# Optimization experiments

Hardware: AMD Instinct MI355X
Metric: run time of the kernel (lower is better)

## Reference

```python
import jax, jax.numpy as jnp
import numpy as np

NUM_BATCH = 8  # GroupNormalization(num_batch=num_groups) with num_groups=8
EPS = 1e-6


def setup_inputs() -> dict:
    key = jax.random.key(0)
    k1, k2, k3 = jax.random.split(key, 3)
    b, h, w, c = 32, 32, 32, 256
    x = jax.random.normal(k1, (b, h, w, c), dtype=jnp.float32)
    gamma = jnp.ones((c,), dtype=jnp.float32)
    beta = jnp.zeros((c,), dtype=jnp.float32)
    w_qkv = jax.random.normal(k2, (c, 3 * c), dtype=jnp.float32) * 0.02
    w_out = jax.random.normal(k3, (c, c), dtype=jnp.float32) * 0.02
    return {"x": x, "gamma": gamma, "beta": beta, "w_qkv": w_qkv, "w_out": w_out}


def reference(x, gamma, beta, w_qkv, w_out):
    b, h, w, c = x.shape
    # --- GroupNormalization (exact quirky semantics of the source) ---
    # num_groups = c // num_batch; reshape to [-1, num_groups, group_size]
    # -> per-(b,h,w)-pixel normalization over contiguous channel groups.
    ng = c // NUM_BATCH          # 32 groups
    gs = c // ng                 # 8 channels per group
    g = x.reshape(-1, ng, gs)
    mu = jnp.mean(g, axis=-1, keepdims=True)
    var = jnp.mean(jnp.square(g - mu), axis=-1, keepdims=True)
    xn = ((g - mu) / jnp.sqrt(var + EPS)).reshape(x.shape)
    xn = gamma * xn + beta
    # --- 1x1 conv to qkv (bias-free) ---
    qkv = jnp.einsum('bhwc,cd->bhwd', xn, w_qkv)  # [b,h,w,3c]
    q, k, v = jnp.split(qkv, 3, axis=-1)
    # self_attention=True branch: tie q=k=v to their mean
    t = (v + q + k) / 3.0
    q = k = v = t
    # --- exact reshapes from the source (raw reshapes, not transposes) ---
    q = jnp.transpose(q, (0, 3, 1, 2)).reshape(b, h * w, c)  # [b,hw,c]
    k = k.reshape(b, c, h * w)                               # [b,c,hw]
    v = jnp.transpose(v, (0, 3, 1, 2)).reshape(b, h * w, c)  # [b,hw,c]
    scores = jnp.matmul(q, k) * (c ** -0.5)                  # [b,hw,hw]
    attn = jax.nn.softmax(scores, axis=-1)
    # NOTE: source passes transpose_a=float (truthy) -> attention is transposed
    out = jnp.matmul(jnp.swapaxes(attn, 1, 2), v)            # [b,hw,c]
    out = out.reshape(b, h, w, c)
    return jnp.einsum('bhwc,cd->bhwd', out, w_out) + x
```

## Files before the change

### kernel.cpp

```cpp
#include <hip/hip_runtime.h>

typedef unsigned short u16;
typedef unsigned char u8;
typedef long long i64;
typedef __bf16 bf16x8 __attribute__((ext_vector_type(8)));
typedef float f32x4 __attribute__((ext_vector_type(4)));
typedef u16 u16x8 __attribute__((ext_vector_type(8)));

#define GLD16(g, l) __builtin_amdgcn_global_load_lds( \
    (const __attribute__((address_space(1))) void*)(g), \
    (__attribute__((address_space(3))) void*)(l), 16, 0, 0)

__device__ __forceinline__ float bf2f(u16 u) {
  return __uint_as_float(((unsigned)u) << 16);
}
__device__ __forceinline__ u16 f2bf(float f) {
  unsigned u = __float_as_uint(f);
  return (u16)((u + 0x7fffu + ((u >> 16) & 1u)) >> 16);
}
__device__ __forceinline__ u8 f8e_sw(float v) {
  unsigned u = __float_as_uint(v);
  unsigned s = (u >> 24) & 0x80u;
  u &= 0x7fffffffu;
  if (u < 0x3c000000u) return (u8)s;
  int b = (int)((u + 0x7FFFFu + ((u >> 20) & 1u)) >> 20) - 960;
  b = b < 8 ? 8 : (b > 126 ? 126 : b);
  return (u8)(b | s);
}
__device__ __forceinline__ float f8d_sw(u8 b) {
  if (!(b & 0x7f)) return 0.0f;
  float v = __uint_as_float((((unsigned)(b & 0x7fu)) << 20) + 0x3C000000u);
  return (b & 0x80u) ? -v : v;
}
__device__ __forceinline__ unsigned pk4(float a, float b, float c, float d) {
#if __has_builtin(__builtin_amdgcn_cvt_pk_fp8_f32)
  int r = __builtin_amdgcn_cvt_pk_fp8_f32(a, b, 0, false);
  r = __builtin_amdgcn_cvt_pk_fp8_f32(c, d, r, true);
  return (unsigned)r;
#else
  return (unsigned)f8e_sw(a) | ((unsigned)f8e_sw(b) << 8) |
         ((unsigned)f8e_sw(c) << 16) | ((unsigned)f8e_sw(d) << 24);
#endif
}
__device__ __forceinline__ float f8df(u8 b) {
#if __has_builtin(__builtin_amdgcn_cvt_f32_fp8)
  return __builtin_amdgcn_cvt_f32_fp8((int)b, 0);
#else
  return f8d_sw(b);
#endif
}
__device__ __forceinline__ int sig(int r) { return (r ^ (r >> 3)) & 7; }

__global__ void combine_w(const float* __restrict__ wqkv, const float* __restrict__ wout,
                          u16* __restrict__ wtT, u16* __restrict__ woutT) {
  int c = blockIdx.x, d = threadIdx.x;
  float t = (wqkv[c * 768 + d] + wqkv[c * 768 + 256 + d] + wqkv[c * 768 + 512 + d]) * (1.0f / 3.0f);
  wtT[d * 256 + c] = f2bf(t);
  woutT[d * 256 + c] = f2bf(wout[c * 256 + d]);
}

__global__ __launch_bounds__(512) void gnT(
    const float* __restrict__ x, const float* __restrict__ gamma,
    const float* __restrict__ beta, const u16* __restrict__ wtT,
    u8* __restrict__ Q8, u8* __restrict__ Kt8) {
  __shared__ u16 lA[2][64 * 64];
  __shared__ u16 lB[2][256 * 64];
  const int m0 = blockIdx.x * 64;
  const int z = m0 >> 10;
  const int t = threadIdx.x, lane = t & 63;
  const int w = t >> 6, wr = w >> 2, wc = w & 3;
  f32x4 acc[2][4] = {};

#define GNT_STAGE(B, K0)                                                        \
  {                                                                             \
    _Pragma("unroll") for (int ch = 0; ch < 4; ch++) {                          \
      int flat = ch * 512 + t, row = flat >> 3, slot = flat & 7;                \
      GLD16(wtT + (size_t)row * 256 + (K0) + (slot ^ sig(row)) * 8,             \
            lB[B] + flat * 8);                                                  \
    }                                                                           \
    int row = t >> 3, grp = t & 7;                                              \
    const float* xp = x + (size_t)(m0 + row) * 256 + (K0) + grp * 8;            \
    float4 a = *(const float4*)xp, b = *(const float4*)(xp + 4);                \
    float mu = (a.x + a.y + a.z + a.w + b.x + b.y + b.z + b.w) * 0.125f;        \
    float d0 = a.x - mu, d1 = a.y - mu, d2 = a.z - mu, d3 = a.w - mu;           \
    float d4 = b.x - mu, d5 = b.y - mu, d6 = b.z - mu, d7 = b.w - mu;           \
    float var = (d0 * d0 + d1 * d1 + d2 * d2 + d3 * d3 +                        \
                 d4 * d4 + d5 * d5 + d6 * d6 + d7 * d7) * 0.125f;               \
    float rs = rsqrtf(var + 1e-6f);                                             \
    const float4 g0 = *(const float4*)(gamma + (K0) + grp * 8);                 \
    const float4 g1 = *(const float4*)(gamma + (K0) + grp * 8 + 4);             \
    const float4 e0 = *(const float4*)(beta + (K0) + grp * 8);                  \
    const float4 e1 = *(const float4*)(beta + (K0) + grp * 8 + 4);              \
    u16x8 o;                                                                    \
    o[0] = f2bf(g0.x * (d0 * rs) + e0.x); o[1] = f2bf(g0.y * (d1 * rs) + e0.y); \
    o[2] = f2bf(g0.z * (d2 * rs) + e0.z); o[3] = f2bf(g0.w * (d3 * rs) + e0.w); \
    o[4] = f2bf(g1.x * (d4 * rs) + e1.x); o[5] = f2bf(g1.y * (d5 * rs) + e1.y); \
    o[6] = f2bf(g1.z * (d6 * rs) + e1.z); o[7] = f2bf(g1.w * (d7 * rs) + e1.w); \
    *(u16x8*)(lA[B] + row * 64 + (grp ^ sig(row)) * 8) = o;                     \
  }

  GNT_STAGE(0, 0);
  __syncthreads();
  for (int it = 0; it < 4; it++) {
    if (it < 3) { GNT_STAGE((it + 1) & 1, (it + 1) * 64); }
    const u16* la = lA[it & 1];
    const u16* lb = lB[it & 1];
#pragma unroll
    for (int kk = 0; kk < 2; kk++) {
      bf16x8 af[2], bfr[4];
#pragma unroll
      for (int mi = 0; mi < 2; mi++) {
        int m = wr * 32 + mi * 16 + (lane & 15);
        af[mi] = *(const bf16x8*)(la + m * 64 + ((kk * 32 + (lane >> 4) * 8) ^ (sig(m) << 3)));
      }
#pragma unroll
      for (int ni = 0; ni < 4; ni++) {
        int n = wc * 64 + ni * 16 + (lane & 15);
        bfr[ni] = *(const bf16x8*)(lb + n * 64 + ((kk * 32 + (lane >> 4) * 8) ^ (sig(n) << 3)));
      }
#pragma unroll
      for (int mi = 0; mi < 2; mi++)
#pragma unroll
        for (int ni = 0; ni < 4; ni++)
          acc[mi][ni] = __builtin_amdgcn_mfma_f32_16x16x32_bf16(af[mi], bfr[ni], acc[mi][ni], 0, 0, 0);
    }
    __syncthreads();
  }

  const int rb = m0 + wr * 32 + ((lane >> 4) << 2);
  const int cb = wc * 64 + (lane & 15);
  u8* kt = (u8*)lB[0];
  u8* qtile = (u8*)lB[1];
#pragma unroll
  for (int mi = 0; mi < 2; mi++)
#pragma unroll
    for (int ni = 0; ni < 4; ni++) {
      int P0 = rb + mi * 16, c = cb + ni * 16;
      int pl = P0 - m0;
      unsigned pk = pk4(acc[mi][ni][0], acc[mi][ni][1], acc[mi][ni][2], acc[mi][ni][3]);
#pragma unroll
      for (int j = 0; j < 4; j++)
        kt[(j * 256 + c) * 16 + (pl >> 2)] = (u8)(pk >> (8 * j));
      *(unsigned*)(qtile + c * 80 + pl) = pk;
    }
  __syncthreads();
  const int ckb = (m0 & 1023) >> 2;
  u8* Kz = Kt8 + (size_t)z * 262144;
  u8* Qz = Q8 + (size_t)z * 262144;
#pragma unroll
  for (int r2 = 0; r2 < 2; r2++) {
    int r = t * 2 + r2;
    uint4 v = *(const uint4*)(kt + r * 16);
    *(uint4*)(Kz + (size_t)r * 256 + ckb) = v;
  }
#pragma unroll
  for (int ph = 0; ph < 2; ph++) {
    int idx = ph * 512 + t, c = idx >> 2, q = idx & 3;
    uint4 v = *(const uint4*)(qtile + c * 80 + q * 16);
    *(uint4*)(Qz + (size_t)c * 1024 + (m0 & 1023) + q * 16) = v;
  }
#undef GNT_STAGE
}

__global__ __launch_bounds__(256) void gemm_s8(
    const u8* __restrict__ Q8, const u8* __restrict__ Kt8,
    u8* __restrict__ Et, float* __restrict__ partials) {
  __shared__ u8 lA[128 * 256];
  __shared__ u8 lB[128 * 256];
  const int z = blockIdx.z;
  const u8* Az = Q8 + (size_t)z * 262144;
  const u8* Bz = Kt8 + (size_t)z * 262144;
  u8* Ez = Et + (size_t)z * 1048576;
  const int m0 = blockIdx.x * 128, n0 = blockIdx.y * 128;
  const int t = threadIdx.x, lane = t & 63;
  const int wr = (t >> 6) >> 1, wc = (t >> 6) & 1;
  f32x4 acc[4][4] = {};

#pragma unroll
  for (int ch = 0; ch < 8; ch++) {
    int flat = ch * 256 + t, row = flat >> 4, slot = flat & 15;
    GLD16(Az + (size_t)(m0 + row) * 256 + (slot ^ sig(row)) * 16, lA + flat * 16);
  }
#pragma unroll
  for (int ch = 0; ch < 8; ch++) {
    int flat = ch * 256 + t, row = flat >> 4, slot = flat & 15;
    GLD16(Bz + (size_t)(n0 + row) * 256 + (slot ^ sig(row)) * 16, lB + flat * 16);
  }
  __syncthreads();
#pragma unroll
  for (int kk = 0; kk < 8; kk++) {
    i64 af[4], bfv[4];
    int koff = kk * 32 + (lane >> 4) * 8;
#pragma unroll
    for (int mi = 0; mi < 4; mi++) {
      int m = wr * 64 + mi * 16 + (lane & 15);
      af[mi] = *(const i64*)(lA + m * 256 + (koff ^ (sig(m) << 4)));
    }
#pragma unroll
    for (int ni = 0; ni < 4; ni++) {
      int n = wc * 64 + ni * 16 + (lane & 15);
      bfv[ni] = *(const i64*)(lB + n * 256 + (koff ^ (sig(n) << 4)));
    }
#pragma unroll
    for (int mi = 0; mi < 4; mi++)
#pragma unroll
      for (int ni = 0; ni < 4; ni++)
        acc[mi][ni] = __builtin_amdgcn_mfma_f32_16x16x32_fp8_fp8(af[mi], bfv[ni], acc[mi][ni], 0, 0, 0);
  }
  __syncthreads();
  u8* ldsC = lA;
  const int rbl = wr * 64 + ((lane >> 4) << 2);
  const int cbl = wc * 64 + (lane & 15);
  const float SCL = 0.0625f * 1.44269504089f;
  float ps[4][4] = {};
#pragma unroll
  for (int mi = 0; mi < 4; mi++)
#pragma unroll
    for (int ni = 0; ni < 4; ni++) {
      int pl = cbl + ni * 16, ib = rbl + mi * 16;
      float e0 = exp2f(acc[mi][ni][0] * SCL);
      float e1 = exp2f(acc[mi][ni][1] * SCL);
      float e2 = exp2f(acc[mi][ni][2] * SCL);
      float e3 = exp2f(acc[mi][ni][3] * SCL);
      ps[mi][0] += e0; ps[mi][1] += e1; ps[mi][2] += e2; ps[mi][3] += e3;
      *(unsigned*)(ldsC + pl * 128 + (ib ^ ((pl & 7) << 4))) = pk4(e0, e1, e2, e3);
    }
#pragma unroll
  for (int mi = 0; mi < 4; mi++)
#pragma unroll
    for (int j = 0; j < 4; j++) {
      float v = ps[mi][j];
      v += __shfl_xor(v, 1); v += __shfl_xor(v, 2);
      v += __shfl_xor(v, 4); v += __shfl_xor(v, 8);
      if ((lane & 15) == 0)
        partials[(size_t)(z * 1024 + m0 + rbl + mi * 16 + j) * 16 + blockIdx.y * 2 + wc] = v;
    }
  __syncthreads();
#pragma unroll
  for (int ph = 0; ph < 4; ph++) {
    int pl = ph * 32 + (t >> 3), ich = (t & 7) * 16;
    uint4 v = *(const uint4*)(ldsC + pl * 128 + (ich ^ ((pl & 7) << 4)));
    *(uint4*)(Ez + (size_t)(n0 + pl) * 1024 + m0 + ich) = v;
  }
}

__global__ __launch_bounds__(256) void qt8(
    const u8* __restrict__ Q8, const float* __restrict__ partials, u8* __restrict__ Qt) {
  __shared__ u8 tile[64][260];
  __shared__ float rv[64];
  const int z = blockIdx.y, i0 = blockIdx.x * 64;
  const u8* src = Q8 + (size_t)z * 262144;
  u8* dst = Qt + (size_t)z * 262144;
  const int t = threadIdx.x;
#pragma unroll
  for (int q = 0; q < 4; q++) {
    uint4 v = *(const uint4*)(src + (size_t)(i0 + (t >> 2)) * 256 + (t & 3) * 64 + q * 16);
    *(uint4*)(&tile[t >> 2][(t & 3) * 64 + q * 16]) = v;
  }
  if (t < 64) {
    const float4* p = (const float4*)(partials + (size_t)(z * 1024 + i0 + t) * 16);
    float4 a = p[0], b = p[1], c = p[2], d = p[3];
    float s = ((a.x + a.y) + (a.z + a.w)) + ((b.x + b.y) + (b.z + b.w)) +
              ((c.x + c.y) + (c.z + c.w)) + ((d.x + d.y) + (d.z + d.w));
    rv[t] = 1024.0f / s;
  }
  __syncthreads();
#pragma unroll
  for (int q = 0; q < 4; q++) {
    unsigned wd[4];
#pragma unroll
    for (int d = 0; d < 4; d++) {
      float f[4];
#pragma unroll
      for (int e = 0; e < 4; e++) {
        int i = q * 16 + d * 4 + e;
        f[e] = f8df(tile[i][t]) * rv[i];
      }
      wd[d] = pk4(f[0], f[1], f[2], f[3]);
    }
    uint4 v = {wd[0], wd[1], wd[2], wd[3]};
    *(uint4*)(dst + (size_t)t * 1024 + i0 + q * 16) = v;
  }
}

__global__ __launch_bounds__(512) void gemm_of(
    const u8* __restrict__ Et, const u8* __restrict__ Qt,
    const u16* __restrict__ woutT, const float* __restrict__ x,
    float* __restrict__ C) {
  __shared__ char smem[131072];
  const int z = blockIdx.y;
  const u8* Az = Et + (size_t)z * 1048576;
  const u8* Bz = Qt + (size_t)z * 262144;
  const int m0 = blockIdx.x * 128;
  const int t = threadIdx.x, lane = t & 63;
  const int w = t >> 6, wr = w >> 2, wc = w & 3;
  f32x4 acc[4][4] = {};

#define O8_STAGE(B, K0)                                                       \
  {                                                                           \
    u8* la_ = (u8*)smem + (B) * 16384;                                        \
    u8* lb_ = (u8*)smem + 32768 + (B) * 32768;                                \
    _Pragma("unroll") for (int ch = 0; ch < 2; ch++) {                        \
      int flat = ch * 512 + t, row = flat >> 3, slot = flat & 7;              \
      GLD16(Az + (size_t)(m0 + row) * 1024 + (K0) + (slot ^ sig(row)) * 16,   \
            la_ + flat * 16);                                                 \
    }                                                                         \
    _Pragma("unroll") for (int ch = 0; ch < 4; ch++) {                        \
      int flat = ch * 512 + t, row = flat >> 3, slot = flat & 7;              \
      GLD16(Bz + (size_t)row * 1024 + (K0) + (slot ^ sig(row)) * 16,          \
            lb_ + flat * 16);                                                 \
    }                                                                         \
  }

  O8_STAGE(0, 0);
  __syncthreads();
  for (int it = 0; it < 8; it++) {
    if (it < 7) { O8_STAGE((it + 1) & 1, (it + 1) * 128); }
    const u8* la = (const u8*)smem + (it & 1) * 16384;
    const u8* lb = (const u8*)smem + 32768 + (it & 1) * 32768;
#pragma unroll
    for (int kk = 0; kk < 4; kk++) {
      i64 af[4], bfv[4];
      int koff = kk * 32 + (lane >> 4) * 8;
#pragma unroll
      for (int mi = 0; mi < 4; mi++) {
        int m = wr * 64 + mi * 16 + (lane & 15);
        af[mi] = *(const i64*)(la + m * 128 + (koff ^ (sig(m) << 4)));
      }
#pragma unroll
      for (int ni = 0; ni < 4; ni++) {
        int n = wc * 64 + ni * 16 + (lane & 15);
        bfv[ni] = *(const i64*)(lb + n * 128 + (koff ^ (sig(n) << 4)));
      }
#pragma unroll
      for (int mi = 0; mi < 4; mi++)
#pragma unroll
        for (int ni = 0; ni < 4; ni++)
          acc[mi][ni] = __builtin_amdgcn_mfma_f32_16x16x32_fp8_fp8(af[mi], bfv[ni], acc[mi][ni], 0, 0, 0);
    }
    __syncthreads();
  }
#undef O8_STAGE

#define W_STAGE(B, K0)                                                        \
  {                                                                           \
    u16* wb_ = (u16*)(smem + 65536 + (B) * 32768);                            \
    _Pragma("unroll") for (int ch = 0; ch < 4; ch++) {                        \
      int flat = ch * 512 + t, row = flat >> 3, slot = flat & 7;              \
      GLD16(woutT + (size_t)row * 256 + (K0) + (slot ^ sig(row)) * 8,         \
            (u8*)wb_ + flat * 16);                                            \
    }                                                                         \
  }
  W_STAGE(0, 0);
  {
    const int rbl = wr * 64 + ((lane >> 4) << 2);
    const int cbl = wc * 64 + (lane & 15);
#pragma unroll
    for (int mi = 0; mi < 4; mi++)
#pragma unroll
      for (int ni = 0; ni < 4; ni++)
#pragma unroll
        for (int j = 0; j < 4; j++) {
          int pl = rbl + mi * 16 + j, c = cbl + ni * 16;
          int byteoff = (pl * 512 + c * 2) ^ ((pl & 7) << 4);
          *(u16*)(smem + byteoff) = f2bf(acc[mi][ni][j] * (1.0f / 1024.0f));
        }
  }
  __syncthreads();

  f32x4 acc2[4][4] = {};
  for (int it2 = 0; it2 < 4; it2++) {
    if (it2 < 3) { W_STAGE((it2 + 1) & 1, (it2 + 1) * 64); }
    const u16* lb = (const u16*)(smem + 65536 + (it2 & 1) * 32768);
#pragma unroll
    for (int kk = 0; kk < 2; kk++) {
      bf16x8 af[4], bfr[4];
#pragma unroll
      for (int mi = 0; mi < 4; mi++) {
        int m = wr * 64 + mi * 16 + (lane & 15);
        int kg = it2 * 64 + kk * 32 + (lane >> 4) * 8;
        af[mi] = *(const bf16x8*)(smem + ((m * 512 + kg * 2) ^ ((m & 7) << 4)));
      }
#pragma unroll
      for (int ni = 0; ni < 4; ni++) {
        int n = wc * 64 + ni * 16 + (lane & 15);
        bfr[ni] = *(const bf16x8*)(lb + n * 64 + ((kk * 32 + (lane >> 4) * 8) ^ (sig(n) << 3)));
      }
#pragma unroll
      for (int mi = 0; mi < 4; mi++)
#pragma unroll
        for (int ni = 0; ni < 4; ni++)
          acc2[mi][ni] = __builtin_amdgcn_mfma_f32_16x16x32_bf16(af[mi], bfr[ni], acc2[mi][ni], 0, 0, 0);
    }
    __syncthreads();
  }
#undef W_STAGE

  const int Pb = z * 1024 + m0 + wr * 64 + ((lane >> 4) << 2);
  const int cb = wc * 64 + (lane & 15);
#pragma unroll
  for (int mi = 0; mi < 4; mi++)
#pragma unroll
    for (int ni = 0; ni < 4; ni++)
#pragma unroll
      for (int j = 0; j < 4; j++) {
        size_t idx = (size_t)(Pb + mi * 16 + j) * 256 + cb + ni * 16;
        C[idx] = acc2[mi][ni][j] + x[idx];
      }
}

extern "C" void kernel_launch(void* const* d_in, const int* in_sizes, int n_in,
                              void* d_out, int out_size, void* d_ws, size_t ws_size,
                              hipStream_t stream) {
  (void)in_sizes; (void)n_in; (void)out_size; (void)ws_size;
  const float* x = (const float*)d_in[0];
  const float* gamma = (const float*)d_in[1];
  const float* beta = (const float*)d_in[2];
  const float* wqkv = (const float*)d_in[3];
  const float* wout = (const float*)d_in[4];
  float* outp = (float*)d_out;

  char* ws = (char*)d_ws;
  const size_t MB = 1024 * 1024;
  u16* wtT = (u16*)(ws + 0);
  u16* woutT = (u16*)(ws + (128 << 10));
  float* partials = (float*)(ws + (512 << 10));
  u8* Q8 = (u8*)(ws + 3 * MB);
  u8* Kt8 = (u8*)(ws + 12 * MB);
  u8* Qt = (u8*)(ws + 21 * MB);
  u8* Et = (u8*)(ws + 30 * MB);

  combine_w<<<256, 256, 0, stream>>>(wqkv, wout, wtT, woutT);
  gnT<<<512, 512, 0, stream>>>(x, gamma, beta, wtT, Q8, Kt8);
  gemm_s8<<<dim3(8, 8, 32), 256, 0, stream>>>(Q8, Kt8, Et, partials);
  qt8<<<dim3(16, 32), 256, 0, stream>>>(Q8, partials, Qt);
  gemm_of<<<dim3(8, 32), 512, 0, stream>>>(Et, Qt, woutT, x, outp);
}
```

Baseline: 102.8 us.

## Reorder grids batch-major, use fine-grained vmcnt waits, and stage epilogue through LDS

Both GEMM kernels now map the batch index to blockIdx.x, so consecutive blocks handle different batches, which changes L2/cache locality across the grid. The main loops of gemm_of replace __syncthreads with explicit vmcnt partial waits plus raw s_barrier. This lets the prefetch of the next stage stay in flight while the current stage is consumed. The final output is staged through LDS so that the residual add and store use coalesced float4 accesses instead of scattered scalar stores. The risk is in the hand-written waitcnt counts: they must match the number of outstanding loads, or the kernel reads stale data.

After: 91.36 us. 1.12x faster.

```diff
diff --git a/kernel.cpp b/kernel.cpp
--- a/kernel.cpp
+++ b/kernel.cpp
@@ -10,6 +10,7 @@
 #define GLD16(g, l) __builtin_amdgcn_global_load_lds( \
     (const __attribute__((address_space(1))) void*)(g), \
     (__attribute__((address_space(3))) void*)(l), 16, 0, 0)
+#define VMW(N) asm volatile("s_waitcnt vmcnt(" #N ")" ::: "memory")
 
 __device__ __forceinline__ float bf2f(u16 u) {
   return __uint_as_float(((unsigned)u) << 16);
@@ -167,11 +168,12 @@
     u8* __restrict__ Et, float* __restrict__ partials) {
   __shared__ u8 lA[128 * 256];
   __shared__ u8 lB[128 * 256];
-  const int z = blockIdx.z;
+  const int z = blockIdx.x;
+  const int mb = blockIdx.y & 7, pb = blockIdx.y >> 3;
   const u8* Az = Q8 + (size_t)z * 262144;
   const u8* Bz = Kt8 + (size_t)z * 262144;
   u8* Ez = Et + (size_t)z * 1048576;
-  const int m0 = blockIdx.x * 128, n0 = blockIdx.y * 128;
+  const int m0 = mb * 128, n0 = pb * 128;
   const int t = threadIdx.x, lane = t & 63;
   const int wr = (t >> 6) >> 1, wc = (t >> 6) & 1;
   f32x4 acc[4][4] = {};
@@ -233,7 +235,7 @@
       v += __shfl_xor(v, 1); v += __shfl_xor(v, 2);
       v += __shfl_xor(v, 4); v += __shfl_xor(v, 8);
       if ((lane & 15) == 0)
-        partials[(size_t)(z * 1024 + m0 + rbl + mi * 16 + j) * 16 + blockIdx.y * 2 + wc] = v;
+        partials[(size_t)(z * 1024 + m0 + rbl + mi * 16 + j) * 16 + pb * 2 + wc] = v;
     }
   __syncthreads();
 #pragma unroll
@@ -288,10 +290,10 @@
     const u16* __restrict__ woutT, const float* __restrict__ x,
     float* __restrict__ C) {
   __shared__ char smem[131072];
-  const int z = blockIdx.y;
+  const int z = blockIdx.x;
+  const int m0 = blockIdx.y * 128;
   const u8* Az = Et + (size_t)z * 1048576;
   const u8* Bz = Qt + (size_t)z * 262144;
-  const int m0 = blockIdx.x * 128;
   const int t = threadIdx.x, lane = t & 63;
   const int w = t >> 6, wr = w >> 2, wc = w & 3;
   f32x4 acc[4][4] = {};
@@ -313,9 +315,16 @@
   }
 
   O8_STAGE(0, 0);
-  __syncthreads();
   for (int it = 0; it < 8; it++) {
-    if (it < 7) { O8_STAGE((it + 1) & 1, (it + 1) * 128); }
+    if (it < 7) {
+      O8_STAGE((it + 1) & 1, (it + 1) * 128);
+      VMW(6);
+    } else {
+      VMW(0);
+    }
+    __builtin_amdgcn_sched_barrier(0);
+    __builtin_amdgcn_s_barrier();
+    __builtin_amdgcn_sched_barrier(0);
     const u8* la = (const u8*)smem + (it & 1) * 16384;
     const u8* lb = (const u8*)smem + 32768 + (it & 1) * 32768;
 #pragma unroll
@@ -338,7 +347,7 @@
         for (int ni = 0; ni < 4; ni++)
           acc[mi][ni] = __builtin_amdgcn_mfma_f32_16x16x32_fp8_fp8(af[mi], bfv[ni], acc[mi][ni], 0, 0, 0);
     }
-    __syncthreads();
+    __builtin_amdgcn_s_barrier();
   }
 #undef O8_STAGE
 
@@ -366,11 +375,22 @@
           *(u16*)(smem + byteoff) = f2bf(acc[mi][ni][j] * (1.0f / 1024.0f));
         }
   }
-  __syncthreads();
+  asm volatile("s_waitcnt lgkmcnt(0)" ::: "memory");
+  __builtin_amdgcn_sched_barrier(0);
+  __builtin_amdgcn_s_barrier();
+  __builtin_amdgcn_sched_barrier(0);
 
   f32x4 acc2[4][4] = {};
   for (int it2 = 0; it2 < 4; it2++) {
-    if (it2 < 3) { W_STAGE((it2 + 1) & 1, (it2 + 1) * 64); }
+    if (it2 < 3) {
+      W_STAGE((it2 + 1) & 1, (it2 + 1) * 64);
+      VMW(4);
+    } else {
+      VMW(0);
+    }
+    __builtin_amdgcn_sched_barrier(0);
+    __builtin_amdgcn_s_barrier();
+    __builtin_amdgcn_sched_barrier(0);
     const u16* lb = (const u16*)(smem + 65536 + (it2 & 1) * 32768);
 #pragma unroll
     for (int kk = 0; kk < 2; kk++) {
@@ -392,21 +412,35 @@
         for (int ni = 0; ni < 4; ni++)
           acc2[mi][ni] = __builtin_amdgcn_mfma_f32_16x16x32_bf16(af[mi], bfr[ni], acc2[mi][ni], 0, 0, 0);
     }
+    __builtin_amdgcn_s_barrier();
+  }
+#undef W_STAGE
+
+  {
+    const int rbl = wr * 64 + ((lane >> 4) << 2);
+    const int cbl = wc * 64 + (lane & 15);
+#pragma unroll
+    for (int mi = 0; mi < 4; mi++)
+#pragma unroll
+      for (int ni = 0; ni < 4; ni++)
+#pragma unroll
+        for (int j = 0; j < 4; j++) {
+          int pl = rbl + mi * 16 + j, c = cbl + ni * 16;
+          *(float*)(smem + ((pl * 1024 + c * 4) ^ ((pl & 7) << 4))) = acc2[mi][ni][j];
+        }
     __syncthreads();
-  }
-#undef W_STAGE
-
-  const int Pb = z * 1024 + m0 + wr * 64 + ((lane >> 4) << 2);
-  const int cb = wc * 64 + (lane & 15);
-#pragma unroll
-  for (int mi = 0; mi < 4; mi++)
-#pragma unroll
-    for (int ni = 0; ni < 4; ni++)
-#pragma unroll
-      for (int j = 0; j < 4; j++) {
-        size_t idx = (size_t)(Pb + mi * 16 + j) * 256 + cb + ni * 16;
-        C[idx] = acc2[mi][ni][j] + x[idx];
-      }
+    const size_t base = (size_t)(z * 1024 + m0) * 256;
+#pragma unroll
+    for (int pi = 0; pi < 16; pi++) {
+      int flat = pi * 512 + t;
+      int row = flat >> 6, ch = flat & 63;
+      f32x4 a = *(const f32x4*)(smem + row * 1024 + ((ch * 16) ^ ((row & 7) << 4)));
+      const float4 xv = *(const float4*)(x + base + (size_t)flat * 4);
+      float4 o;
+      o.x = a[0] + xv.x; o.y = a[1] + xv.y; o.z = a[2] + xv.z; o.w = a[3] + xv.w;
+      *(float4*)(C + base + (size_t)flat * 4) = o;
+    }
+  }
 }
 
 extern "C" void kernel_launch(void* const* d_in, const int* in_sizes, int n_in,
@@ -432,7 +466,7 @@
 
   combine_w<<<256, 256, 0, stream>>>(wqkv, wout, wtT, woutT);
   gnT<<<512, 512, 0, stream>>>(x, gamma, beta, wtT, Q8, Kt8);
-  gemm_s8<<<dim3(8, 8, 32), 256, 0, stream>>>(Q8, Kt8, Et, partials);
+  gemm_s8<<<dim3(32, 64), 256, 0, stream>>>(Q8, Kt8, Et, partials);
   qt8<<<dim3(16, 32), 256, 0, stream>>>(Q8, partials, Qt);
-  gemm_of<<<dim3(8, 32), 512, 0, stream>>>(Et, Qt, woutT, x, outp);
-}
+  gemm_of<<<dim3(32, 8), 512, 0, stream>>>(Et, Qt, woutT, x, outp);
+}
```
